# Kernel optimization log

Hardware: AMD Instinct MI355X
Metric: run time of the kernel (lower is better)

## Reference

```python
import jax, jax.numpy as jnp
import numpy as np

B, S, NH, HD = 2, 2048, 32, 128     # batch seqs, tokens per seq, heads, head_dim
H = NH * HD                          # hidden = 4096
BLOCK = 64                           # paged KV-cache block size
NBLK = S // BLOCK                    # blocks per sequence
NUM_BLOCKS = B * NBLK                # total cache blocks


def alibi_slopes(n):
    # n is a power of two: slope_i = 2^(-8*(i+1)/n)
    return np.asarray([2.0 ** (-8.0 * (i + 1) / n) for i in range(n)], dtype=np.float32)


def setup_inputs() -> dict:
    key = jax.random.key(0)
    k1, k2, k3 = jax.random.split(key, 3)
    hidden_states = jax.random.normal(k1, (B * S, H), jnp.float32)
    w_pack = jax.random.normal(k2, (H, 3 * H), jnp.float32) * 0.02
    o_proj_w = jax.random.normal(k3, (H, H), jnp.float32) * 0.02
    k_cache = jnp.zeros((NUM_BLOCKS, BLOCK, NH, HD), jnp.float32)
    v_cache = jnp.zeros((NUM_BLOCKS, BLOCK, NH, HD), jnp.float32)
    block_offsets = jnp.arange(NUM_BLOCKS, dtype=jnp.int32).reshape(B, NBLK)
    return {
        "hidden_states": hidden_states,
        "w_pack": w_pack,
        "o_proj_w": o_proj_w,
        "k_cache": k_cache,
        "v_cache": v_cache,
        "block_offsets": block_offsets,
    }


def reference(hidden_states, w_pack, o_proj_w, k_cache, v_cache, block_offsets):
    # fused QKV projection, chunk(3, -1)
    qkv = hidden_states @ w_pack                      # [B*S, 3H]
    q, k, v = jnp.split(qkv, 3, axis=-1)
    q = q.reshape(B, S, NH, HD)
    k = k.reshape(B, NBLK, BLOCK, NH, HD)
    v = v.reshape(B, NBLK, BLOCK, NH, HD)

    # fill_kv_cache: scatter new K/V into paged cache blocks
    k_cache = k_cache.at[block_offsets].set(k)        # [NUM_BLOCKS, BLOCK, NH, HD]
    v_cache = v_cache.at[block_offsets].set(v)

    # paged read: gather non-contiguous blocks back per sequence
    kg = k_cache[block_offsets].reshape(B, S, NH, HD)
    vg = v_cache[block_offsets].reshape(B, S, NH, HD)

    slopes = jnp.asarray(alibi_slopes(NH))            # [NH]
    scale = 1.0 / jnp.sqrt(jnp.float32(HD))
    scores = jnp.einsum('bqhd,bkhd->bhqk', q, kg) * scale   # [B,NH,S,S]
    pos = jnp.arange(S)
    # ALiBi bias: slope * key_position (row-shift invariant under softmax)
    scores = scores + slopes[None, :, None, None] * pos[None, None, None, :]
    causal = pos[:, None] >= pos[None, :]             # [S,S]
    scores = jnp.where(causal[None, None], scores, jnp.float32(-1e30))
    probs = jax.nn.softmax(scores, axis=-1)
    attn = jnp.einsum('bhqk,bkhd->bqhd', probs, vg).reshape(B * S, H)
    return attn @ o_proj_w
```

## Files before the change

### kernel.cpp

```cpp
#include <hip/hip_runtime.h>
#include <hip/hip_bf16.h>
#include <stdint.h>

typedef __attribute__((ext_vector_type(4))) float f32x4;
typedef __attribute__((ext_vector_type(8))) __bf16 bf16x8;
typedef __attribute__((ext_vector_type(8))) unsigned short u16x8;
typedef __attribute__((ext_vector_type(4))) unsigned short u16x4;
typedef __attribute__((ext_vector_type(4))) unsigned int u32x4;

#define GLL16(g, l) __builtin_amdgcn_global_load_lds( \
    (const __attribute__((address_space(1))) unsigned int*)(uintptr_t)(g), \
    (__attribute__((address_space(3))) unsigned int*)(uintptr_t)(l), 16, 0, 0)

__device__ __forceinline__ unsigned short bf16u(float f) {
  return __builtin_bit_cast(unsigned short, __float2bfloat16(f));
}

#define PB 2
#define PS 2048
#define PNH 32
#define PHD 128
#define PH 4096
#define P3H 12288

__global__ __launch_bounds__(256)
void cvt_f32_bf16(const float* __restrict__ in, unsigned short* __restrict__ out, int n) {
  int stride = gridDim.x * blockDim.x;
  for (int i = blockIdx.x * blockDim.x + threadIdx.x; i * 8 < n; i += stride) {
    int base = i * 8;
    f32x4 a = *(const f32x4*)(in + base);
    f32x4 b = *(const f32x4*)(in + base + 4);
    u16x8 o;
#pragma unroll
    for (int j = 0; j < 4; ++j) { o[j] = bf16u(a[j]); o[4 + j] = bf16u(b[j]); }
    *(u16x8*)(out + base) = o;
  }
}

__global__ __launch_bounds__(256)
void transpose_cvt(const float* __restrict__ in, unsigned short* __restrict__ out,
                   int K, int N) {
  __shared__ __align__(16) unsigned short tile[64][68];
  int k0 = blockIdx.y * 64, n0 = blockIdx.x * 64;
  int t = threadIdx.x;
  int rr = t >> 4, cc = (t & 15) * 4;
#pragma unroll
  for (int p = 0; p < 4; ++p) {
    int r = rr + p * 16;
    f32x4 v = *(const f32x4*)(in + (size_t)(k0 + r) * N + n0 + cc);
    u16x4 w;
#pragma unroll
    for (int j = 0; j < 4; ++j) w[j] = bf16u(v[j]);
    *(u16x4*)&tile[r][cc] = w;
  }
  __syncthreads();
#pragma unroll
  for (int p = 0; p < 4; ++p) {
    int nl = rr + p * 16;
    u16x4 w;
#pragma unroll
    for (int j = 0; j < 4; ++j) w[j] = tile[cc + j][nl];
    *(u16x4*)(out + (size_t)(n0 + nl) * K + k0 + cc) = w;
  }
}

#define STAGE16(TT) do { int sb_ = ((TT) & 3) << 15; \
    GLL16(aSrc + (size_t)(TT) * 32, smem + sb_ + (wave << 10)); \
    GLL16(bSrc + (size_t)(TT) * 32, smem + sb_ + 16384 + (wave << 10)); } while (0)

#define TILE16(T, DOSTAGE, VM, DOBAR) do { \
    char* cb_ = smem + (((T) & 3) << 15); \
    if (DOSTAGE) STAGE16((T) + 3); \
    bf16x8 av[4], bv[4]; \
    _Pragma("unroll") \
    for (int j = 0; j < 4; ++j) \
      bv[j] = *(const bf16x8*)(cb_ + 16384 + (((wn << 6) + (j << 4) + lr) << 6) + lchunk); \
    _Pragma("unroll") \
    for (int i = 0; i < 4; ++i) \
      av[i] = *(const bf16x8*)(cb_ + (((wm << 6) + (i << 4) + lr) << 6) + lchunk); \
    __builtin_amdgcn_s_setprio(1); \
    _Pragma("unroll") \
    for (int i = 0; i < 4; ++i) \
      _Pragma("unroll") \
      for (int j = 0; j < 4; ++j) \
        acc[i][j] = __builtin_amdgcn_mfma_f32_16x16x32_bf16(av[i], bv[j], acc[i][j], 0, 0, 0); \
    __builtin_amdgcn_s_setprio(0); \
    if ((VM) == 4)      asm volatile("s_waitcnt vmcnt(4)" ::: "memory"); \
    else if ((VM) == 2) asm volatile("s_waitcnt vmcnt(2)" ::: "memory"); \
    else if ((VM) == 0) asm volatile("s_waitcnt vmcnt(0)" ::: "memory"); \
    if (DOBAR) __builtin_amdgcn_s_barrier(); \
  } while (0)

template<int OUTF32>
__global__ __launch_bounds__(1024, 4)
void gemm256(const unsigned short* __restrict__ A, const unsigned short* __restrict__ Bt,
             void* __restrict__ Cv, int M, int N, int K) {
  __shared__ __align__(16) char smem[131072];
  const int tid = threadIdx.x;
  const int wave = tid >> 6, lane = tid & 63;
  const int lr = lane & 15, lg = lane >> 4;
  const int wm = wave >> 2, wn = wave & 3;
  const int lchunk = (lg ^ ((lr >> 1) & 3)) << 4;
  const int nbn = N >> 8;
  const int nbm = M >> 8;
  int bid = blockIdx.x;
  const int bnx = nbn >> 3;
  int x = bid & 7;
  int l = bid >> 3;
  int bm = l % nbm;
  int bn = x * bnx + l / nbm;
  const size_t arow = (size_t)bm << 8;
  const size_t brow = (size_t)bn << 8;

  const int srow = (wave << 4) + (lane >> 2);
  const int scol = ((lane & 3) ^ ((lane >> 3) & 3)) << 3;
  const unsigned short* aSrc = A  + (arow + srow) * K + scol;
  const unsigned short* bSrc = Bt + (brow + srow) * K + scol;

  f32x4 acc[4][4] = {};

  STAGE16(0); STAGE16(1); STAGE16(2);
  asm volatile("s_waitcnt vmcnt(4)" ::: "memory");
  __builtin_amdgcn_s_barrier();

  for (int t = 0; t < 125; ++t) TILE16(t, 1, 4, 1);
  TILE16(125, 0, 2, 1);
  TILE16(126, 0, 0, 1);
  TILE16(127, 0, -1, 0);

  int crow = (bm << 8) + (wm << 6) + (lg << 2);
  int ccol = (bn << 8) + (wn << 6) + lr;
#pragma unroll
  for (int i = 0; i < 4; ++i)
#pragma unroll
    for (int j = 0; j < 4; ++j)
#pragma unroll
      for (int r = 0; r < 4; ++r) {
        size_t off = (size_t)(crow + (i << 4) + r) * N + ccol + (j << 4);
        if (OUTF32) ((float*)Cv)[off] = acc[i][j][r];
        else        ((unsigned short*)Cv)[off] = bf16u(acc[i][j][r]);
      }
}

__global__ __launch_bounds__(512, 2)
void attn_kernel(const unsigned short* __restrict__ qkv, unsigned short* __restrict__ out) {
  __shared__ __align__(16) unsigned short Ks[2][64 * 128];
  __shared__ __align__(16) unsigned short Vt[128 * 64];
  __shared__ __align__(16) unsigned short Ps[8][32 * 72];
  int tid = threadIdx.x, wave = tid >> 6, lane = tid & 63;
  int lr = lane & 15, lg = lane >> 4;
  int idx = blockIdx.x;
  int qtsel = idx & 7, h = (idx >> 3) & 31, bsel = idx >> 8;
  int qt = bsel ? qtsel : 7 - qtsel;
  size_t rb = (size_t)bsel * PS;
  int qcol = h << 7, kcol = PH + (h << 7), vcol = 2 * PH + (h << 7);
  int q0 = (qt << 8) + (wave << 5);

  bf16x8 aq[2][4];
#pragma unroll
  for (int qs = 0; qs < 2; ++qs)
#pragma unroll
    for (int f = 0; f < 4; ++f)
      aq[qs][f] = *(const bf16x8*)(qkv + (rb + q0 + (qs << 4) + lr) * P3H + qcol + (f << 5) + (lg << 3));

  float m_run[2][4], l_run[2][4];
#pragma unroll
  for (int qs = 0; qs < 2; ++qs)
#pragma unroll
    for (int r = 0; r < 4; ++r) { m_run[qs][r] = -1e30f; l_run[qs][r] = 0.f; }
  f32x4 acc_o[2][8] = {};

  float slope2 = __builtin_amdgcn_exp2f(-(float)(h + 1) * 0.25f) * 1.44269504f;
  const float scale2 = 0.08838834764831845f * 1.44269504f;

  char* KsB = (char*)Ks;
  char* VtB = (char*)Vt;
  const int kk0 = (tid & 31) << 1;
  const int d0 = (tid >> 5) << 3;

  {
    size_t krow = rb;
#pragma unroll
    for (int i = 0; i < 2; ++i) {
      int pf = (wave << 11) | (i << 10) | (lane << 4);
      int row = pf >> 8;
      int lch = ((pf >> 4) & 15) ^ (row & 7);
      GLL16(qkv + (krow + row) * P3H + kcol + (lch << 3), KsB + (wave << 11) + (i << 10));
    }
  }
  u32x4 vr0 = *(const u32x4*)(qkv + (rb + kk0 + 0) * P3H + vcol + d0);
  u32x4 vr1 = *(const u32x4*)(qkv + (rb + kk0 + 1) * P3H + vcol + d0);

  const int tmax = 4 * qt + 3;
  for (int t = 0; t <= tmax; ++t) {
    int cur = t & 1;
    char* KsCur = KsB + (cur << 14);
    char* KsNxt = KsB + ((cur ^ 1) << 14);
    bool more = (t < tmax);

    u32x4 nv0 = {}, nv1 = {};
    if (more) {
      size_t krow = rb + ((size_t)(t + 1) << 6);
#pragma unroll
      for (int i = 0; i < 2; ++i) {
        int pf = (wave << 11) | (i << 10) | (lane << 4);
        int row = pf >> 8;
        int lch = ((pf >> 4) & 15) ^ (row & 7);
        GLL16(qkv + (krow + row) * P3H + kcol + (lch << 3), KsNxt + (wave << 11) + (i << 10));
      }
      nv0 = *(const u32x4*)(qkv + (krow + kk0 + 0) * P3H + vcol + d0);
      nv1 = *(const u32x4*)(qkv + (krow + kk0 + 1) * P3H + vcol + d0);
    }

    if (more) asm volatile("s_waitcnt vmcnt(4)" ::: "memory");
    else      asm volatile("s_waitcnt vmcnt(0)" ::: "memory");

    {
      const unsigned short* e0 = (const unsigned short*)&vr0;
      const unsigned short* e1 = (const unsigned short*)&vr1;
#pragma unroll
      for (int j = 0; j < 8; ++j) {
        int d = d0 + j;
        unsigned int w = (unsigned int)e0[j] | ((unsigned int)e1[j] << 16);
        int byteoff = ((d << 7) + (kk0 << 1)) ^ ((d & 7) << 4);
        *(unsigned int*)(VtB + byteoff) = w;
      }
    }
    asm volatile("s_waitcnt lgkmcnt(0)" ::: "memory");
    __builtin_amdgcn_s_barrier();

    f32x4 sc[2][4];
    __builtin_amdgcn_s_setprio(1);
#pragma unroll
    for (int f = 0; f < 4; ++f) {
      f32x4 c0 = {}, c1 = {};
#pragma unroll
      for (int ks = 0; ks < 4; ++ks) {
        int kkr = (f << 4) + lr;
        int ch = (lg + (ks << 2)) ^ (kkr & 7);
        bf16x8 bk = *(const bf16x8*)(KsCur + (kkr << 8) + (ch << 4));
        c0 = __builtin_amdgcn_mfma_f32_16x16x32_bf16(aq[0][ks], bk, c0, 0, 0, 0);
        c1 = __builtin_amdgcn_mfma_f32_16x16x32_bf16(aq[1][ks], bk, c1, 0, 0, 0);
      }
      sc[0][f] = c0; sc[1][f] = c1;
    }
    __builtin_amdgcn_s_setprio(0);

    int kvb = t << 6;
    bool needmask = (kvb + 63 > q0);
#pragma unroll
    for (int qs = 0; qs < 2; ++qs) {
      float vals[4][4];
#pragma unroll
      for (int f = 0; f < 4; ++f) {
        int kv = kvb + (f << 4) + lr;
        float bias = slope2 * (float)kv;
#pragma unroll
        for (int r = 0; r < 4; ++r) {
          float v = sc[qs][f][r] * scale2 + bias;
          if (needmask && kv > q0 + (qs << 4) + (lg << 2) + r) v = -1e30f;
          vals[r][f] = v;
        }
      }
      float alpha[4];
#pragma unroll
      for (int r = 0; r < 4; ++r) {
        float mr = fmaxf(fmaxf(vals[r][0], vals[r][1]), fmaxf(vals[r][2], vals[r][3]));
#pragma unroll
        for (int d2 = 1; d2 < 16; d2 <<= 1) mr = fmaxf(mr, __shfl_xor(mr, d2, 16));
        float mnew = fmaxf(m_run[qs][r], mr);
        alpha[r] = __builtin_amdgcn_exp2f(m_run[qs][r] - mnew);
        m_run[qs][r] = mnew;
      }
#pragma unroll
      for (int r = 0; r < 4; ++r) {
        float s = 0.f;
#pragma unroll
        for (int f = 0; f < 4; ++f) {
          float p = __builtin_amdgcn_exp2f(vals[r][f] - m_run[qs][r]);
          s += p;
          Ps[wave][((qs << 4) + (lg << 2) + r) * 72 + (f << 4) + lr] = bf16u(p);
        }
        l_run[qs][r] = l_run[qs][r] * alpha[r] + s;
      }
#pragma unroll
      for (int d = 0; d < 8; ++d) {
        f32x4 a4 = acc_o[qs][d];
#pragma unroll
        for (int r = 0; r < 4; ++r) a4[r] *= alpha[r];
        acc_o[qs][d] = a4;
      }
    }

    bf16x8 pa[2][2];
#pragma unroll
    for (int qs = 0; qs < 2; ++qs)
#pragma unroll
      for (int ks = 0; ks < 2; ++ks)
        pa[qs][ks] = *(const bf16x8*)((char*)&Ps[wave][0] + ((qs << 4) + lr) * 144 + (ks << 6) + (lg << 4));
    __builtin_amdgcn_s_setprio(1);
#pragma unroll
    for (int d = 0; d < 8; ++d) {
#pragma unroll
      for (int ks = 0; ks < 2; ++ks) {
        int dr = (d << 4) + lr;
        int ch = (lg + (ks << 2)) ^ (dr & 7);
        bf16x8 bv = *(const bf16x8*)(VtB + (dr << 7) + (ch << 4));
        acc_o[0][d] = __builtin_amdgcn_mfma_f32_16x16x32_bf16(pa[0][ks], bv, acc_o[0][d], 0, 0, 0);
        acc_o[1][d] = __builtin_amdgcn_mfma_f32_16x16x32_bf16(pa[1][ks], bv, acc_o[1][d], 0, 0, 0);
      }
    }
    __builtin_amdgcn_s_setprio(0);
    __builtin_amdgcn_s_barrier();

    if (more) { vr0 = nv0; vr1 = nv1; }
  }

#pragma unroll
  for (int qs = 0; qs < 2; ++qs) {
    float rinv[4];
#pragma unroll
    for (int r = 0; r < 4; ++r) {
      float s = l_run[qs][r];
#pragma unroll
      for (int d2 = 1; d2 < 16; d2 <<= 1) s += __shfl_xor(s, d2, 16);
      rinv[r] = 1.f / s;
    }
#pragma unroll
    for (int d = 0; d < 8; ++d)
#pragma unroll
      for (int r = 0; r < 4; ++r) {
        float o = acc_o[qs][d][r] * rinv[r];
        out[(rb + q0 + (qs << 4) + (lg << 2) + r) * PH + (h << 7) + (d << 4) + lr] = bf16u(o);
      }
  }
}

extern "C" void kernel_launch(void* const* d_in, const int* in_sizes, int n_in,
                              void* d_out, int out_size, void* d_ws, size_t ws_size,
                              hipStream_t stream) {
  const float* hidden = (const float*)d_in[0];
  const float* w_pack = (const float*)d_in[1];
  const float* o_proj = (const float*)d_in[2];

  char* ws = (char*)d_ws;
  unsigned short* wpackT = (unsigned short*)(ws);
  unsigned short* qkv    = (unsigned short*)(ws + 100663296);
  unsigned short* oprojT = (unsigned short*)(ws + 201326592);
  unsigned short* hbf    = (unsigned short*)(ws + 234881024);
  unsigned short* attnb  = hbf;

  int M = PB * PS;

  cvt_f32_bf16<<<2048, 256, 0, stream>>>(hidden, hbf, M * PH);
  transpose_cvt<<<dim3(P3H / 64, PH / 64), 256, 0, stream>>>(w_pack, wpackT, PH, P3H);
  transpose_cvt<<<dim3(PH / 64, PH / 64), 256, 0, stream>>>(o_proj, oprojT, PH, PH);
  gemm256<0><<<(M / 256) * (P3H / 256), 1024, 0, stream>>>(hbf, wpackT, qkv, M, P3H, PH);
  attn_kernel<<<PB * PNH * (PS / 256), 512, 0, stream>>>(qkv, attnb);
  gemm256<1><<<(M / 256) * (PH / 256), 1024, 0, stream>>>(attnb, oprojT, d_out, M, PH, PH);
}
```

Baseline: 737.3 us.

## Restructure GEMM to 8 waves with 128x64 per-wave tiles and ping-pong scheduling

The 256x256 GEMM moves from 16 waves with 64x64 warp tiles and a 4-stage, K=32 pipeline to 8 waves, each owning a 128x64 output tile. It uses a double-buffered K=64 pipeline whose staging is split into quarter-tile loads interleaved with four MFMA sub-phases. Barriers separate the phases, and the LDS swizzle is updated for 128-byte rows. The aim is more MFMA work per LDS read and overlap of global loads with compute. The cost is more accumulator registers per wave (128 floats), more barriers per K-step, and fewer waves available to hide latency.

```diff
diff --git a/kernel.cpp b/kernel.cpp
--- a/kernel.cpp
+++ b/kernel.cpp
@@ -64,35 +64,71 @@
   }
 }
 
-#define STAGE16(TT) do { int sb_ = ((TT) & 3) << 15; \
-    GLL16(aSrc + (size_t)(TT) * 32, smem + sb_ + (wave << 10)); \
-    GLL16(bSrc + (size_t)(TT) * 32, smem + sb_ + 16384 + (wave << 10)); } while (0)
-
-#define TILE16(T, DOSTAGE, VM, DOBAR) do { \
-    char* cb_ = smem + (((T) & 3) << 15); \
-    if (DOSTAGE) STAGE16((T) + 3); \
-    bf16x8 av[4], bv[4]; \
+#define STAGEHT(T, OP, H) do { \
+    const unsigned short* s_ = (OP) ? bS : aS; \
+    char* d_ = smem + (((T) & 1) << 16) + ((OP) << 15) + ((H) << 14) + (wave << 10); \
+    GLL16(s_ + ((size_t)((H) << 7)) * K + (size_t)(T) * 64, d_); \
+    GLL16(s_ + ((size_t)(((H) << 7) + 64)) * K + (size_t)(T) * 64, d_ + 8192); \
+  } while (0)
+
+#define RD_AV8(RI, BUFA) do { \
     _Pragma("unroll") \
-    for (int j = 0; j < 4; ++j) \
-      bv[j] = *(const bf16x8*)(cb_ + 16384 + (((wn << 6) + (j << 4) + lr) << 6) + lchunk); \
+    for (int i_ = 0; i_ < 4; ++i_) { \
+      av[2 * i_]     = *(const bf16x8*)((BUFA) + ((RI) << 13) + (i_ << 11) + (lr << 7) + ch0); \
+      av[2 * i_ + 1] = *(const bf16x8*)((BUFA) + ((RI) << 13) + (i_ << 11) + (lr << 7) + (ch0 ^ 64)); \
+    } } while (0)
+
+#define RD_BV4(CI, BUFB, DST) do { \
     _Pragma("unroll") \
-    for (int i = 0; i < 4; ++i) \
-      av[i] = *(const bf16x8*)(cb_ + (((wm << 6) + (i << 4) + lr) << 6) + lchunk); \
-    __builtin_amdgcn_s_setprio(1); \
+    for (int j_ = 0; j_ < 2; ++j_) { \
+      DST[2 * j_]     = *(const bf16x8*)((BUFB) + ((CI) << 12) + (j_ << 11) + (lr << 7) + ch0); \
+      DST[2 * j_ + 1] = *(const bf16x8*)((BUFB) + ((CI) << 12) + (j_ << 11) + (lr << 7) + (ch0 ^ 64)); \
+    } } while (0)
+
+#define MFMA16(RI, CI, BV) do { \
     _Pragma("unroll") \
-    for (int i = 0; i < 4; ++i) \
+    for (int i_ = 0; i_ < 4; ++i_) \
       _Pragma("unroll") \
-      for (int j = 0; j < 4; ++j) \
-        acc[i][j] = __builtin_amdgcn_mfma_f32_16x16x32_bf16(av[i], bv[j], acc[i][j], 0, 0, 0); \
-    __builtin_amdgcn_s_setprio(0); \
-    if ((VM) == 4)      asm volatile("s_waitcnt vmcnt(4)" ::: "memory"); \
-    else if ((VM) == 2) asm volatile("s_waitcnt vmcnt(2)" ::: "memory"); \
+      for (int j_ = 0; j_ < 2; ++j_) { \
+        acc[(RI) * 4 + i_][(CI) * 2 + j_] = __builtin_amdgcn_mfma_f32_16x16x32_bf16(av[2 * i_],     BV[2 * j_],     acc[(RI) * 4 + i_][(CI) * 2 + j_], 0, 0, 0); \
+        acc[(RI) * 4 + i_][(CI) * 2 + j_] = __builtin_amdgcn_mfma_f32_16x16x32_bf16(av[2 * i_ + 1], BV[2 * j_ + 1], acc[(RI) * 4 + i_][(CI) * 2 + j_], 0, 0, 0); \
+      } } while (0)
+
+#define TILE8(T, S1, S3, S4, VM) do { \
+    char* bufA_ = smem + (((T) & 1) << 16) + (wm << 14); \
+    char* bufB_ = smem + (((T) & 1) << 16) + 32768 + ((wn >> 1) << 14) + ((wn & 1) << 13); \
+     \
+    RD_AV8(0, bufA_); \
+    RD_BV4(0, bufB_, bv0); \
+    if (S1) STAGEHT((T) + 1, 1, 1); \
+    __builtin_amdgcn_s_barrier(); \
+    asm volatile("s_waitcnt lgkmcnt(0)" ::: "memory"); \
+    __builtin_amdgcn_s_setprio(1); MFMA16(0, 0, bv0); __builtin_amdgcn_s_setprio(0); \
+    __builtin_amdgcn_s_barrier(); \
+     \
+    RD_BV4(1, bufB_, bv1); \
+    __builtin_amdgcn_s_barrier(); \
+    asm volatile("s_waitcnt lgkmcnt(0)" ::: "memory"); \
+    __builtin_amdgcn_s_setprio(1); MFMA16(0, 1, bv1); __builtin_amdgcn_s_setprio(0); \
+    __builtin_amdgcn_s_barrier(); \
+     \
+    RD_AV8(1, bufA_); \
+    if (S3) STAGEHT((T) + 2, 1, 0); \
+    __builtin_amdgcn_s_barrier(); \
+    asm volatile("s_waitcnt lgkmcnt(0)" ::: "memory"); \
+    __builtin_amdgcn_s_setprio(1); MFMA16(1, 0, bv0); __builtin_amdgcn_s_setprio(0); \
+    __builtin_amdgcn_s_barrier(); \
+     \
+    if (S4) { STAGEHT((T) + 2, 0, 0); STAGEHT((T) + 2, 0, 1); } \
+    __builtin_amdgcn_s_barrier(); \
+    __builtin_amdgcn_s_setprio(1); MFMA16(1, 1, bv1); __builtin_amdgcn_s_setprio(0); \
+    if ((VM) == 6)      asm volatile("s_waitcnt vmcnt(6)" ::: "memory"); \
     else if ((VM) == 0) asm volatile("s_waitcnt vmcnt(0)" ::: "memory"); \
-    if (DOBAR) __builtin_amdgcn_s_barrier(); \
+    __builtin_amdgcn_s_barrier(); \
   } while (0)
 
 template<int OUTF32>
-__global__ __launch_bounds__(1024, 4)
+__global__ __launch_bounds__(512, 2)
 void gemm256(const unsigned short* __restrict__ A, const unsigned short* __restrict__ Bt,
              void* __restrict__ Cv, int M, int N, int K) {
   __shared__ __align__(16) char smem[131072];
@@ -100,7 +136,7 @@
   const int wave = tid >> 6, lane = tid & 63;
   const int lr = lane & 15, lg = lane >> 4;
   const int wm = wave >> 2, wn = wave & 3;
-  const int lchunk = (lg ^ ((lr >> 1) & 3)) << 4;
+  const int ch0 = ((lg ^ (lr & 7)) << 4);
   const int nbn = N >> 8;
   const int nbm = M >> 8;
   int bid = blockIdx.x;
@@ -112,26 +148,27 @@
   const size_t arow = (size_t)bm << 8;
   const size_t brow = (size_t)bn << 8;
 
-  const int srow = (wave << 4) + (lane >> 2);
-  const int scol = ((lane & 3) ^ ((lane >> 3) & 3)) << 3;
-  const unsigned short* aSrc = A  + (arow + srow) * K + scol;
-  const unsigned short* bSrc = Bt + (brow + srow) * K + scol;
-
-  f32x4 acc[4][4] = {};
-
-  STAGE16(0); STAGE16(1); STAGE16(2);
-  asm volatile("s_waitcnt vmcnt(4)" ::: "memory");
+  const int sg = lane >> 3;
+  const int scolE = ((lane & 7) ^ sg) << 3;
+  const unsigned short* aS = A  + (arow + (wave << 3) + sg) * (size_t)K + scolE;
+  const unsigned short* bS = Bt + (brow + (wave << 3) + sg) * (size_t)K + scolE;
+
+  f32x4 acc[8][4] = {};
+  bf16x8 av[8], bv0[4], bv1[4];
+
+  STAGEHT(0, 0, 0); STAGEHT(0, 0, 1); STAGEHT(0, 1, 0); STAGEHT(0, 1, 1);
+  STAGEHT(1, 1, 0); STAGEHT(1, 0, 0); STAGEHT(1, 0, 1);
+  asm volatile("s_waitcnt vmcnt(6)" ::: "memory");
   __builtin_amdgcn_s_barrier();
 
-  for (int t = 0; t < 125; ++t) TILE16(t, 1, 4, 1);
-  TILE16(125, 0, 2, 1);
-  TILE16(126, 0, 0, 1);
-  TILE16(127, 0, -1, 0);
-
-  int crow = (bm << 8) + (wm << 6) + (lg << 2);
+  for (int t = 0; t < 62; ++t) TILE8(t, 1, 1, 1, 6);
+  TILE8(62, 1, 0, 0, 0);
+  TILE8(63, 0, 0, 0, -1);
+
+  int crow = (bm << 8) + (wm << 7) + (lg << 2);
   int ccol = (bn << 8) + (wn << 6) + lr;
 #pragma unroll
-  for (int i = 0; i < 4; ++i)
+  for (int i = 0; i < 8; ++i)
 #pragma unroll
     for (int j = 0; j < 4; ++j)
 #pragma unroll
@@ -355,7 +392,7 @@
   cvt_f32_bf16<<<2048, 256, 0, stream>>>(hidden, hbf, M * PH);
   transpose_cvt<<<dim3(P3H / 64, PH / 64), 256, 0, stream>>>(w_pack, wpackT, PH, P3H);
   transpose_cvt<<<dim3(PH / 64, PH / 64), 256, 0, stream>>>(o_proj, oprojT, PH, PH);
-  gemm256<0><<<(M / 256) * (P3H / 256), 1024, 0, stream>>>(hbf, wpackT, qkv, M, P3H, PH);
+  gemm256<0><<<(M / 256) * (P3H / 256), 512, 0, stream>>>(hbf, wpackT, qkv, M, P3H, PH);
   attn_kernel<<<PB * PNH * (PS / 256), 512, 0, stream>>>(qkv, attnb);
-  gemm256<1><<<(M / 256) * (PH / 256), 1024, 0, stream>>>(attnb, oprojT, d_out, M, PH, PH);
-}
+  gemm256<1><<<(M / 256) * (PH / 256), 512, 0, stream>>>(attnb, oprojT, d_out, M, PH, PH);
+}
```

Measured after the change: 710.1 us (median of 2 runs). 3.7% less time.
